# Kernel tuning notes

Hardware: AMD Instinct MI355X
Metric: run time of the kernel (lower is better)

## Reference

```python
import jax, jax.numpy as jnp
import numpy as np

NUM_EXPERTS = 8
NUM_SLOTS = 4

def setup_inputs() -> dict:
    key = jax.random.key(0)
    k1, k2 = jax.random.split(key)
    B, S, D = 8, 4096, 1024
    x = jax.random.normal(k1, (B, S, D), dtype=jnp.float32)
    W_phi = jax.random.normal(k2, (D, NUM_EXPERTS * NUM_SLOTS), dtype=jnp.float32) * (1.0 / np.sqrt(D))
    b_phi = jnp.zeros((NUM_EXPERTS * NUM_SLOTS,), dtype=jnp.float32)
    return {"x": x, "W_phi": W_phi, "b_phi": b_phi}

def reference(x, W_phi, b_phi):
    B, S, D = x.shape
    E, P = NUM_EXPERTS, NUM_SLOTS
    # phi logits: (B, S, E, P)
    phi_logits = (jnp.einsum('bsd,dk->bsk', x, W_phi) + b_phi).reshape(B, S, E, P)
    # softmax over seq axis (dispatch weights)
    phi_weights = jax.nn.softmax(phi_logits, axis=1)
    # soft slots: weighted sum of tokens per (expert, slot) -> (B, E, P, D)
    # (faithful to expand_dims*multiply*sum-over-seq in the original, fused as einsum)
    soft_slots = jnp.einsum('bsep,bsd->bepd', phi_weights, x)
    expert_inputs = soft_slots.reshape(B, E, P * D)
    expert_weights = jnp.full((B, S, E), 1.0 / E, dtype=x.dtype)
    expert_indices = jnp.broadcast_to(jnp.arange(E, dtype=jnp.int32)[None, None, :], (B, S, E))
    raw_gate_probs = jax.nn.softmax(phi_logits, axis=-1)
    return (expert_weights, expert_indices, phi_weights, soft_slots, expert_inputs, phi_logits, raw_gate_probs)
```

## Files before the change

kernel.cpp:

```cpp
#include <hip/hip_runtime.h>
#include <hip/hip_bf16.h>

#define BB 8
#define SS 4096
#define DD 1024
#define KK 32
#define EE 8
#define PP 4

#define O0 0L
#define O1 262144L
#define O2 524288L
#define O3 1572864L
#define O4 1835008L
#define O5 2097152L
#define O6 3145728L

#define WA 0L
#define WB 8192L
#define WPKH 16384L
#define WPKL 32768L
#define WC 49152L

typedef __attribute__((ext_vector_type(8))) short short8v;
typedef __attribute__((ext_vector_type(4))) float f32x4;

__device__ __forceinline__ unsigned short f2bf(float f) {
    unsigned u = __builtin_bit_cast(unsigned, f);
    unsigned r = (u + 0x7FFFu + ((u >> 16) & 1u)) >> 16;
    return (unsigned short)r;
}
__device__ __forceinline__ float bf2f(unsigned short h) {
    return __builtin_bit_cast(float, (unsigned)h << 16);
}

__global__ __launch_bounds__(256) void k_wprep(const float* __restrict__ Wp,
    unsigned short* __restrict__ wh, unsigned short* __restrict__ wl)
{
    const int t  = blockIdx.x * 256 + threadIdx.x;
    const int l  = t & 63;
    const int tt = (t >> 6) & 1;
    const int ks = t >> 7;
    const int col = tt * 16 + (l & 15);
    const int dbase = ks * 32 + (l >> 4) * 8;
    const long obase = ((long)(ks * 2 + tt) * 64 + l) * 8;
#pragma unroll
    for (int j = 0; j < 8; ++j) {
        const float w = Wp[(long)(dbase + j) * KK + col];
        const unsigned short h = f2bf(w);
        const float lo = w - bf2f(h);
        wh[obase + j] = h;
        wl[obase + j] = f2bf(lo);
    }
}

__global__ __launch_bounds__(256) void k_logits_mfma(const float* __restrict__ x,
    const unsigned short* __restrict__ wh, const unsigned short* __restrict__ wl,
    float* __restrict__ wsP)
{
    const int tid  = threadIdx.x;
    const int wv   = tid >> 6;
    const int lane = tid & 63;
    const int blk  = blockIdx.x;
    const int tile = blk >> 1, half = blk & 1;
    const long tokw = (long)tile * 64 + wv * 16;
    const int mrow = lane & 15;
    const int kg   = lane >> 4;

    const float* xr = x + (tokw + mrow) * DD + half * 512 + kg * 8;
    const uint4* bh = reinterpret_cast<const uint4*>(wh) + (long)half * 16 * 2 * 64 + lane;
    const uint4* bl = reinterpret_cast<const uint4*>(wl) + (long)half * 16 * 2 * 64 + lane;

    f32x4 acc0 = {0.f, 0.f, 0.f, 0.f};
    f32x4 acc1 = {0.f, 0.f, 0.f, 0.f};

#pragma unroll 4
    for (int s = 0; s < 16; ++s) {
        const float4 u0 = *reinterpret_cast<const float4*>(xr + s * 32);
        const float4 u1 = *reinterpret_cast<const float4*>(xr + s * 32 + 4);
        const short8v b0h = __builtin_bit_cast(short8v, bh[(long)(s * 2    ) * 64]);
        const short8v b1h = __builtin_bit_cast(short8v, bh[(long)(s * 2 + 1) * 64]);
        const short8v b0l = __builtin_bit_cast(short8v, bl[(long)(s * 2    ) * 64]);
        const short8v b1l = __builtin_bit_cast(short8v, bl[(long)(s * 2 + 1) * 64]);

        const float xf[8] = {u0.x, u0.y, u0.z, u0.w, u1.x, u1.y, u1.z, u1.w};
        short8v ah, al;
#pragma unroll
        for (int j = 0; j < 8; ++j) {
            const unsigned short h = f2bf(xf[j]);
            ah[j] = (short)h;
            al[j] = (short)f2bf(xf[j] - bf2f(h));
        }
        acc0 = __builtin_amdgcn_mfma_f32_16x16x32_bf16(ah, b0h, acc0, 0, 0, 0);
        acc1 = __builtin_amdgcn_mfma_f32_16x16x32_bf16(ah, b1h, acc1, 0, 0, 0);
        acc0 = __builtin_amdgcn_mfma_f32_16x16x32_bf16(al, b0h, acc0, 0, 0, 0);
        acc1 = __builtin_amdgcn_mfma_f32_16x16x32_bf16(al, b1h, acc1, 0, 0, 0);
        acc0 = __builtin_amdgcn_mfma_f32_16x16x32_bf16(ah, b0l, acc0, 0, 0, 0);
        acc1 = __builtin_amdgcn_mfma_f32_16x16x32_bf16(ah, b1l, acc1, 0, 0, 0);
    }

#pragma unroll
    for (int r = 0; r < 4; ++r) {
        const long tok = tokw + kg * 4 + r;
        float* o = wsP + ((long)half * 32768 + tok) * KK + mrow;
        o[0]  = acc0[r];
        o[16] = acc1[r];
    }
}

__global__ __launch_bounds__(256) void k_comb2(const float* __restrict__ wsP,
    const float* __restrict__ bp, float* __restrict__ out, float* __restrict__ ws)
{
    const int blk = blockIdx.x;
    const int tid = threadIdx.x;
    const int wv  = __builtin_amdgcn_readfirstlane(tid >> 6);
    const long g  = (long)blk * 256 + tid;
    float acc[KK];
#pragma unroll
    for (int k = 0; k < KK; ++k) acc[k] = bp[k];
#pragma unroll
    for (int h = 0; h < 2; ++h) {
        const float4* p = reinterpret_cast<const float4*>(wsP + ((long)h * 32768 + g) * KK);
#pragma unroll
        for (int m = 0; m < 8; ++m) {
            const float4 v = p[m];
            acc[4*m]   += v.x;
            acc[4*m+1] += v.y;
            acc[4*m+2] += v.z;
            acc[4*m+3] += v.w;
        }
    }
    float4* pl = reinterpret_cast<float4*>(out + O5 + g * KK);
#pragma unroll
    for (int m = 0; m < 8; ++m)
        pl[m] = make_float4(acc[4*m], acc[4*m+1], acc[4*m+2], acc[4*m+3]);
    float rg[KK];
#pragma unroll
    for (int e = 0; e < EE; ++e) {
        const float mx = fmaxf(fmaxf(acc[4*e], acc[4*e+1]), fmaxf(acc[4*e+2], acc[4*e+3]));
        float s = 0.f;
#pragma unroll
        for (int p = 0; p < PP; ++p) { rg[4*e+p] = __expf(acc[4*e+p] - mx); s += rg[4*e+p]; }
        const float ri = 1.f / s;
#pragma unroll
        for (int p = 0; p < PP; ++p) rg[4*e+p] *= ri;
    }
    float4* prg = reinterpret_cast<float4*>(out + O6 + g * KK);
#pragma unroll
    for (int m = 0; m < 8; ++m)
        prg[m] = make_float4(rg[4*m], rg[4*m+1], rg[4*m+2], rg[4*m+3]);
    float4* pew = reinterpret_cast<float4*>(out + O0 + g * EE);
    pew[0] = make_float4(0.125f, 0.125f, 0.125f, 0.125f);
    pew[1] = make_float4(0.125f, 0.125f, 0.125f, 0.125f);
    float4* pei = reinterpret_cast<float4*>(out + O1 + g * EE);
    pei[0] = make_float4(0.f, 1.f, 2.f, 3.f);
    pei[1] = make_float4(4.f, 5.f, 6.f, 7.f);

    float m[KK];
#pragma unroll
    for (int k = 0; k < KK; ++k) m[k] = acc[k];
    for (int off = 1; off < 64; off <<= 1) {
#pragma unroll
        for (int k = 0; k < KK; ++k) m[k] = fmaxf(m[k], __shfl_xor(m[k], off));
    }
    __shared__ float lm[4][KK];
    __shared__ float lsum[4][KK];
    if ((tid & 63) == 0) {
#pragma unroll
        for (int k = 0; k < KK; ++k) lm[wv][k] = m[k];
    }
    __syncthreads();
#pragma unroll
    for (int k = 0; k < KK; ++k)
        m[k] = fmaxf(fmaxf(lm[0][k], lm[1][k]), fmaxf(lm[2][k], lm[3][k]));
    float sv[KK];
#pragma unroll
    for (int k = 0; k < KK; ++k) sv[k] = __expf(acc[k] - m[k]);
    for (int off = 1; off < 64; off <<= 1) {
#pragma unroll
        for (int k = 0; k < KK; ++k) sv[k] += __shfl_xor(sv[k], off);
    }
    if ((tid & 63) == 0) {
#pragma unroll
        for (int k = 0; k < KK; ++k) lsum[wv][k] = sv[k];
    }
    __syncthreads();
    if (tid == 0) {
#pragma unroll
        for (int k = 0; k < KK; ++k) {
            ws[WA + (long)blk * 64 + k]      = m[k];
            ws[WA + (long)blk * 64 + 32 + k] = lsum[0][k] + lsum[1][k] + lsum[2][k] + lsum[3][k];
        }
    }
}

__global__ __launch_bounds__(256) void k_logits4(const float* __restrict__ x,
    const float* __restrict__ Wp, const float* __restrict__ bp,
    float* __restrict__ out)
{
    __shared__ float xl[2][64][68];
    __shared__ float wl[2][64][32];
    const int tid  = threadIdx.x;
    const int wv   = __builtin_amdgcn_readfirstlane(tid >> 6);
    const int lane = tid & 63;
    const long tok0 = (long)blockIdx.x * 64;
    const long g   = tok0 + lane;
    const int sr = tid >> 2;
    const int sco = (tid & 3) * 4;
    float acc[8];
#pragma unroll
    for (int j = 0; j < 8; ++j) acc[j] = 0.f;
    float4 xr[4], wr[2];
#pragma unroll
    for (int j = 0; j < 4; ++j)
        xr[j] = *reinterpret_cast<const float4*>(x + (tok0 + sr) * DD + sco + j * 16);
#pragma unroll
    for (int j = 0; j < 2; ++j)
        wr[j] = *reinterpret_cast<const float4*>(Wp + tid * 8 + j * 4);
#pragma unroll
    for (int j = 0; j < 4; ++j)
        *reinterpret_cast<float4*>(&xl[0][sr][sco + j * 16]) = xr[j];
#pragma unroll
    for (int j = 0; j < 2; ++j)
        *reinterpret_cast<float4*>(&wl[0][0][0] + tid * 8 + j * 4) = wr[j];
    __syncthreads();
    for (int c = 0; c < 16; ++c) {
        const int cb = c & 1;
        if (c < 15) {
            const long dg = (long)(c + 1) * 64;
#pragma unroll
            for (int j = 0; j < 4; ++j)
                xr[j] = *reinterpret_cast<const float4*>(
                    x + (tok0 + sr) * DD + dg + sco + j * 16);
#pragma unroll
            for (int j = 0; j < 2; ++j)
                wr[j] = *reinterpret_cast<const float4*>(Wp + dg * KK + tid * 8 + j * 4);
        }
        const float* xb = &xl[cb][lane][0];
        const float* wb = &wl[cb][0][0] + wv * 8;
#pragma unroll 4
        for (int dq = 0; dq < 16; ++dq) {
            const float4 xv = *reinterpret_cast<const float4*>(xb + dq * 4);
#pragma unroll
            for (int dd = 0; dd < 4; ++dd) {
                const float xs = (dd == 0) ? xv.x : (dd == 1) ? xv.y
                               : (dd == 2) ? xv.z : xv.w;
                const float4 w0 = *reinterpret_cast<const float4*>(wb + (dq * 4 + dd) * 32);
                const float4 w1 = *reinterpret_cast<const float4*>(wb + (dq * 4 + dd) * 32 + 4);
                acc[0] = fmaf(xs, w0.x, acc[0]);
                acc[1] = fmaf(xs, w0.y, acc[1]);
                acc[2] = fmaf(xs, w0.z, acc[2]);
                acc[3] = fmaf(xs, w0.w, acc[3]);
                acc[4] = fmaf(xs, w1.x, acc[4]);
                acc[5] = fmaf(xs, w1.y, acc[5]);
                acc[6] = fmaf(xs, w1.z, acc[6]);
                acc[7] = fmaf(xs, w1.w, acc[7]);
            }
        }
        if (c < 15) {
#pragma unroll
            for (int j = 0; j < 4; ++j)
                *reinterpret_cast<float4*>(&xl[cb ^ 1][sr][sco + j * 16]) = xr[j];
#pragma unroll
            for (int j = 0; j < 2; ++j)
                *reinterpret_cast<float4*>(&wl[cb ^ 1][0][0] + tid * 8 + j * 4) = wr[j];
        }
        __syncthreads();
    }
#pragma unroll
    for (int j = 0; j < 8; ++j) acc[j] += bp[wv * 8 + j];
    float* o5 = out + O5 + g * KK + wv * 8;
    *reinterpret_cast<float4*>(o5)     = make_float4(acc[0], acc[1], acc[2], acc[3]);
    *reinterpret_cast<float4*>(o5 + 4) = make_float4(acc[4], acc[5], acc[6], acc[7]);
    float rg[8];
#pragma unroll
    for (int e = 0; e < 2; ++e) {
        const float* aa = &acc[e * 4];
        const float m = fmaxf(fmaxf(aa[0], aa[1]), fmaxf(aa[2], aa[3]));
        float s = 0.f;
#pragma unroll
        for (int p = 0; p < PP; ++p) { rg[e*4+p] = __expf(aa[p] - m); s += rg[e*4+p]; }
        const float ri = 1.f / s;
#pragma unroll
        for (int p = 0; p < PP; ++p) rg[e*4+p] *= ri;
    }
    float* o6 = out + O6 + g * KK + wv * 8;
    *reinterpret_cast<float4*>(o6)     = make_float4(rg[0], rg[1], rg[2], rg[3]);
    *reinterpret_cast<float4*>(o6 + 4) = make_float4(rg[4], rg[5], rg[6], rg[7]);
    if (wv == 0) {
        float4* p = reinterpret_cast<float4*>(out + O0 + g * EE);
        p[0] = make_float4(0.125f, 0.125f, 0.125f, 0.125f);
        p[1] = make_float4(0.125f, 0.125f, 0.125f, 0.125f);
    } else if (wv == 1) {
        float4* p = reinterpret_cast<float4*>(out + O1 + g * EE);
        p[0] = make_float4(0.f, 1.f, 2.f, 3.f);
        p[1] = make_float4(4.f, 5.f, 6.f, 7.f);
    }
}

__global__ __launch_bounds__(256) void k_smpart(const float* __restrict__ out,
                                                float* __restrict__ ws)
{
    const int blk = blockIdx.x;
    const int tid = threadIdx.x;
    const int wv  = __builtin_amdgcn_readfirstlane(tid >> 6);
    const int b = blk >> 4, sc = blk & 15;
    const long s  = (long)sc * 256 + tid;
    const float* row = out + O5 + ((long)b * SS + s) * KK;
    float v[KK];
    const float4* r4 = reinterpret_cast<const float4*>(row);
#pragma unroll
    for (int q = 0; q < 8; ++q) {
        const float4 t = r4[q];
        v[4*q] = t.x; v[4*q+1] = t.y; v[4*q+2] = t.z; v[4*q+3] = t.w;
    }
    float m[KK];
#pragma unroll
    for (int k = 0; k < KK; ++k) m[k] = v[k];
    for (int off = 1; off < 64; off <<= 1) {
#pragma unroll
        for (int k = 0; k < KK; ++k) m[k] = fmaxf(m[k], __shfl_xor(m[k], off));
    }
    __shared__ float lm[4][KK];
    __shared__ float lsum[4][KK];
    if ((tid & 63) == 0) {
#pragma unroll
        for (int k = 0; k < KK; ++k) lm[wv][k] = m[k];
    }
    __syncthreads();
#pragma unroll
    for (int k = 0; k < KK; ++k)
        m[k] = fmaxf(fmaxf(lm[0][k], lm[1][k]), fmaxf(lm[2][k], lm[3][k]));
    float sv[KK];
#pragma unroll
    for (int k = 0; k < KK; ++k) sv[k] = __expf(v[k] - m[k]);
    for (int off = 1; off < 64; off <<= 1) {
#pragma unroll
        for (int k = 0; k < KK; ++k) sv[k] += __shfl_xor(sv[k], off);
    }
    if ((tid & 63) == 0) {
#pragma unroll
        for (int k = 0; k < KK; ++k) lsum[wv][k] = sv[k];
    }
    __syncthreads();
    if (tid == 0) {
#pragma unroll
        for (int k = 0; k < KK; ++k) {
            ws[WA + (long)blk * 64 + k]      = m[k];
            ws[WA + (long)blk * 64 + 32 + k] = lsum[0][k] + lsum[1][k] + lsum[2][k] + lsum[3][k];
        }
    }
}

__global__ __launch_bounds__(256) void k_smcomb(float* __restrict__ ws)
{
    const int tid = threadIdx.x;
    const int b = tid >> 5, k = tid & 31;
    float m = -1e30f, s = 0.f;
    for (int c = 0; c < 16; ++c) {
        const float mc = ws[WA + (long)(b * 16 + c) * 64 + k];
        const float sc = ws[WA + (long)(b * 16 + c) * 64 + 32 + k];
        const float nm = fmaxf(m, mc);
        s = s * __expf(m - nm) + sc * __expf(mc - nm);
        m = nm;
    }
    ws[WB + (long)b * 64 + k]      = m;
    ws[WB + (long)b * 64 + 32 + k] = 1.f / s;
}

__global__ __launch_bounds__(256) void k_slots2pw(const float* __restrict__ x,
    float* __restrict__ out, const float* __restrict__ ws,
    float* __restrict__ dst, int SC, int SLEN)
{
    __shared__ float pwl[2][64 * KK];
    const int tid = threadIdx.x;
    const int blk = blockIdx.x;
    const int sc  = blk % SC;
    const int t2  = blk / SC;
    const int dc  = t2 & 3;
    const int b   = t2 >> 2;
    const int d   = dc * 256 + tid;
    const int k0  = (tid & 3) * 8;

    float km[8], krv[8];
#pragma unroll
    for (int j = 0; j < 8; ++j) {
        km[j]  = ws[WB + (long)b * 64 + k0 + j];
        krv[j] = ws[WB + (long)b * 64 + 32 + k0 + j];
    }

    float acc[KK];
#pragma unroll
    for (int k = 0; k < KK; ++k) acc[k] = 0.f;
    const long s0 = (long)sc * SLEN;
    const float* lg = out + O5 + ((long)b * SS + s0) * KK;
    float* o2       = out + O2 + ((long)b * SS + s0) * KK;
    const float* xp = x + ((long)b * SS + s0) * DD + d;
    const int NCH = SLEN >> 6;

    float4 r0 = *reinterpret_cast<const float4*>(lg + tid * 8);
    float4 r1 = *reinterpret_cast<const float4*>(lg + tid * 8 + 4);
    {
        const float4 t0 = make_float4(__expf(r0.x - km[0]) * krv[0],
                                      __expf(r0.y - km[1]) * krv[1],
                                      __expf(r0.z - km[2]) * krv[2],
                                      __expf(r0.w - km[3]) * krv[3]);
        const float4 t1 = make_float4(__expf(r1.x - km[4]) * krv[4],
                                      __expf(r1.y - km[5]) * krv[5],
                                      __expf(r1.z - km[6]) * krv[6],
                                      __expf(r1.w - km[7]) * krv[7]);
        *reinterpret_cast<float4*>(&pwl[0][tid * 8])     = t0;
        *reinterpret_cast<float4*>(&pwl[0][tid * 8 + 4]) = t1;
        if (dc == 0) {
            *reinterpret_cast<float4*>(o2 + tid * 8)     = t0;
            *reinterpret_cast<float4*>(o2 + tid * 8 + 4) = t1;
        }
    }
    __syncthreads();

    for (int ch = 0; ch < NCH; ++ch) {
        const int cb = ch & 1;
        if (ch + 1 < NCH) {
            const float* ln = lg + (long)(ch + 1) * 64 * KK;
            r0 = *reinterpret_cast<const float4*>(ln + tid * 8);
            r1 = *reinterpret_cast<const float4*>(ln + tid * 8 + 4);
        }
        const float* xc = xp + (long)ch * 64 * DD;
        const float* pb = &pwl[cb][0];
#pragma unroll 8
        for (int i = 0; i < 64; ++i) {
            const float xv = xc[(long)i * DD];
#pragma unroll
            for (int q = 0; q < 8; ++q) {
                const float4 w = *reinterpret_cast<const float4*>(pb + i * KK + q * 4);
                acc[4*q]   = fmaf(w.x, xv, acc[4*q]);
                acc[4*q+1] = fmaf(w.y, xv, acc[4*q+1]);
                acc[4*q+2] = fmaf(w.z, xv, acc[4*q+2]);
                acc[4*q+3] = fmaf(w.w, xv, acc[4*q+3]);
            }
        }
        if (ch + 1 < NCH) {
            const float4 t0 = make_float4(__expf(r0.x - km[0]) * krv[0],
                                          __expf(r0.y - km[1]) * krv[1],
                                          __expf(r0.z - km[2]) * krv[2],
                                          __expf(r0.w - km[3]) * krv[3]);
            const float4 t1 = make_float4(__expf(r1.x - km[4]) * krv[4],
                                          __expf(r1.y - km[5]) * krv[5],
                                          __expf(r1.z - km[6]) * krv[6],
                                          __expf(r1.w - km[7]) * krv[7]);
            *reinterpret_cast<float4*>(&pwl[cb ^ 1][tid * 8])     = t0;
            *reinterpret_cast<float4*>(&pwl[cb ^ 1][tid * 8 + 4]) = t1;
            if (dc == 0) {
                float* on = o2 + (long)(ch + 1) * 64 * KK;
                *reinterpret_cast<float4*>(on + tid * 8)     = t0;
                *reinterpret_cast<float4*>(on + tid * 8 + 4) = t1;
            }
        }
        __syncthreads();
    }
    float* o = dst + ((long)(sc * BB + b) * KK) * DD + d;
#pragma unroll
    for (int k = 0; k < KK; ++k) o[(long)k * DD] = acc[k];
}

__global__ __launch_bounds__(256) void k_red(const float* __restrict__ src,
                                             float* __restrict__ out, int SC)
{
    const long i4 = (long)blockIdx.x * 256 + threadIdx.x;
    float4 s = make_float4(0.f, 0.f, 0.f, 0.f);
    const float4* p = reinterpret_cast<const float4*>(src);
    for (int c = 0; c < SC; ++c) {
        const float4 t = p[(long)c * 65536 + i4];
        s.x += t.x; s.y += t.y; s.z += t.z; s.w += t.w;
    }
    reinterpret_cast<float4*>(out + O3)[i4] = s;
    reinterpret_cast<float4*>(out + O4)[i4] = s;
}

extern "C" void kernel_launch(void* const* d_in, const int* in_sizes, int n_in,
                              void* d_out, int out_size, void* d_ws, size_t ws_size,
                              hipStream_t stream)
{
    const float* x  = (const float*)d_in[0];
    const float* Wp = (const float*)d_in[1];
    const float* bp = (const float*)d_in[2];
    float* out = (float*)d_out;
    float* ws  = (float*)d_ws;

    const size_t wfloats = ws_size / 4;
    const long wsP_floats = 2L * 32768 * KK;
    const bool mfma_ok = wfloats >= (size_t)(WC + wsP_floats);

    if (mfma_ok) {
        unsigned short* wh = (unsigned short*)(ws + WPKH);
        unsigned short* wl = (unsigned short*)(ws + WPKL);
        hipLaunchKernelGGL(k_wprep,       dim3(16),   dim3(256), 0, stream, Wp, wh, wl);
        hipLaunchKernelGGL(k_logits_mfma, dim3(1024), dim3(256), 0, stream, x, wh, wl, ws + WC);
        hipLaunchKernelGGL(k_comb2,       dim3(128),  dim3(256), 0, stream, ws + WC, bp, out, ws);
    } else {
        hipLaunchKernelGGL(k_logits4, dim3(512), dim3(256), 0, stream, x, Wp, bp, out);
        hipLaunchKernelGGL(k_smpart,  dim3(128), dim3(256), 0, stream, out, ws);
    }

    hipLaunchKernelGGL(k_smcomb, dim3(1), dim3(256), 0, stream, ws);

    int SC = 0;
    if      (wfloats >= (size_t)(WC + 16L * 262144)) SC = 16;
    else if (wfloats >= (size_t)(WC +  8L * 262144)) SC = 8;
    else if (wfloats >= (size_t)(WC +  4L * 262144)) SC = 4;
    else if (wfloats >= (size_t)(WC +  2L * 262144)) SC = 2;
    else if (wfloats >= (size_t)(WC +  1L * 262144)) SC = 1;

    if (SC >= 1) {
        hipLaunchKernelGGL(k_slots2pw, dim3(BB * 4 * SC), dim3(256), 0, stream,
                           x, out, ws, ws + WC, SC, SS / SC);
        hipLaunchKernelGGL(k_red, dim3(256), dim3(256), 0, stream, ws + WC, out, SC);
    } else {
        hipLaunchKernelGGL(k_slots2pw, dim3(BB * 4), dim3(256), 0, stream,
                           x, out, ws, out + O3, 1, SS);
        hipLaunchKernelGGL(k_red, dim3(256), dim3(256), 0, stream, out + O3, out, 1);
    }
}
```

Baseline: 108.7 us.

## Compute soft-slot weighted sums with split-bf16 MFMA using prepacked phi-weight fragments

Adds a kernel that finishes the sequence softmax, writes phi_weights, and packs them into hi/lo bf16 MFMA fragment layouts. A new slots kernel then computes the weighted token sums with 16x16x32 bf16 MFMAs, using a three-term hi/lo split to keep near-fp32 accuracy. This replaces the scalar FMA slots kernel and the single-block softmax-combine kernel on the main path. The cost is an extra fragment-pack pass, more workspace, and three MFMA products per tile, with some risk of accuracy loss.

```diff
diff --git a/kernel.cpp b/kernel.cpp
--- a/kernel.cpp
+++ b/kernel.cpp
@@ -20,7 +20,9 @@
 #define WB 8192L
 #define WPKH 16384L
 #define WPKL 32768L
-#define WC 49152L
+#define PWFH 49152L
+#define PWFL 573440L
+#define WC2 1097728L
 
 typedef __attribute__((ext_vector_type(8))) short short8v;
 typedef __attribute__((ext_vector_type(4))) float f32x4;
@@ -192,6 +194,125 @@
             ws[WA + (long)blk * 64 + 32 + k] = lsum[0][k] + lsum[1][k] + lsum[2][k] + lsum[3][k];
         }
     }
+}
+
+__global__ __launch_bounds__(256) void k_pwfrag(float* __restrict__ out,
+    const float* __restrict__ ws, unsigned short* __restrict__ fh,
+    unsigned short* __restrict__ fl)
+{
+    const int blk = blockIdx.x;
+    const int b  = blk >> 7;
+    const int t  = threadIdx.x;
+    const int h  = t >> 7;
+    const int l  = (t >> 1) & 63;
+    const int jh = t & 1;
+    const int k  = h * 16 + (l & 15);
+    const long sbase = (long)(blk & 127) * 32 + ((l >> 4) << 3) + jh * 4;
+
+    float m = -1e30f, s = 0.f;
+#pragma unroll
+    for (int c = 0; c < 16; ++c) {
+        const float mc = ws[WA + (long)(b * 16 + c) * 64 + k];
+        const float sc = ws[WA + (long)(b * 16 + c) * 64 + 32 + k];
+        const float nm = fmaxf(m, mc);
+        s = s * __expf(m - nm) + sc * __expf(mc - nm);
+        m = nm;
+    }
+    const float rv = 1.f / s;
+
+    unsigned short hh[4], ll[4];
+#pragma unroll
+    for (int j2 = 0; j2 < 4; ++j2) {
+        const long sg = (long)b * SS + sbase + j2;
+        const float lg = out[O5 + sg * KK + k];
+        const float pw = __expf(lg - m) * rv;
+        out[O2 + sg * KK + k] = pw;
+        const unsigned u = __builtin_bit_cast(unsigned, pw);
+        hh[j2] = (unsigned short)(u >> 16);
+        const float hi = __builtin_bit_cast(float, u & 0xFFFF0000u);
+        ll[j2] = (unsigned short)(__builtin_bit_cast(unsigned, pw - hi) >> 16);
+    }
+    const long fb = (((long)blk * 2 + h) * 64 + l) * 8 + jh * 4;
+    *reinterpret_cast<uint2*>(fh + fb) =
+        make_uint2((unsigned)hh[0] | ((unsigned)hh[1] << 16),
+                   (unsigned)hh[2] | ((unsigned)hh[3] << 16));
+    *reinterpret_cast<uint2*>(fl + fb) =
+        make_uint2((unsigned)ll[0] | ((unsigned)ll[1] << 16),
+                   (unsigned)ll[2] | ((unsigned)ll[3] << 16));
+}
+
+__global__ __launch_bounds__(256) void k_slots_mfma(const float* __restrict__ x,
+    const unsigned short* __restrict__ fh, const unsigned short* __restrict__ fl,
+    float* __restrict__ dst, int SC, int SLEN)
+{
+    const int tid  = threadIdx.x;
+    const int wv   = tid >> 6;
+    const int lane = tid & 63;
+    const int blk  = blockIdx.x;
+    const int sc   = blk % SC;
+    const int t2   = blk / SC;
+    const int dt   = t2 & 15;
+    const int b    = t2 >> 4;
+    const int d0   = dt * 64 + wv * 16;
+    const int n    = lane & 15;
+    const int kg   = lane >> 4;
+    const int CPS  = SLEN >> 5;
+
+    const float* xb = x + ((long)b * SS + (long)sc * SLEN) * DD + d0 + n;
+    const uint4* FH = reinterpret_cast<const uint4*>(fh);
+    const uint4* FL = reinterpret_cast<const uint4*>(fl);
+
+    f32x4 a0 = {0.f, 0.f, 0.f, 0.f};
+    f32x4 a1 = {0.f, 0.f, 0.f, 0.f};
+
+#pragma unroll 2
+    for (int c = 0; c < CPS; ++c) {
+        float xf[8];
+#pragma unroll
+        for (int j = 0; j < 8; ++j)
+            xf[j] = xb[(long)(c * 32 + kg * 8 + j) * DD];
+        short8v xh, xl;
+#pragma unroll
+        for (int j = 0; j < 8; ++j) {
+            const unsigned u = __builtin_bit_cast(unsigned, xf[j]);
+            xh[j] = (short)(u >> 16);
+            const float hi = __builtin_bit_cast(float, u & 0xFFFF0000u);
+            xl[j] = (short)(__builtin_bit_cast(unsigned, xf[j] - hi) >> 16);
+        }
+        const long fidx = ((long)(b * 128 + sc * CPS + c) * 2) * 64 + lane;
+        const short8v p0h = __builtin_bit_cast(short8v, FH[fidx]);
+        const short8v p0l = __builtin_bit_cast(short8v, FL[fidx]);
+        const short8v p1h = __builtin_bit_cast(short8v, FH[fidx + 64]);
+        const short8v p1l = __builtin_bit_cast(short8v, FL[fidx + 64]);
+
+        a0 = __builtin_amdgcn_mfma_f32_16x16x32_bf16(p0h, xh, a0, 0, 0, 0);
+        a1 = __builtin_amdgcn_mfma_f32_16x16x32_bf16(p1h, xh, a1, 0, 0, 0);
+        a0 = __builtin_amdgcn_mfma_f32_16x16x32_bf16(p0l, xh, a0, 0, 0, 0);
+        a1 = __builtin_amdgcn_mfma_f32_16x16x32_bf16(p1l, xh, a1, 0, 0, 0);
+        a0 = __builtin_amdgcn_mfma_f32_16x16x32_bf16(p0h, xl, a0, 0, 0, 0);
+        a1 = __builtin_amdgcn_mfma_f32_16x16x32_bf16(p1h, xl, a1, 0, 0, 0);
+    }
+
+    float* ob = dst + ((long)(sc * BB + b) * KK) * DD + d0 + n;
+#pragma unroll
+    for (int r = 0; r < 4; ++r) {
+        ob[(long)((kg << 2) + r) * DD]        = a0[r];
+        ob[(long)(16 + (kg << 2) + r) * DD]   = a1[r];
+    }
+}
+
+__global__ __launch_bounds__(256) void k_red(const float* __restrict__ src,
+                                             float* __restrict__ out, int SC)
+{
+    const long i4 = (long)blockIdx.x * 256 + threadIdx.x;
+    float4 s = make_float4(0.f, 0.f, 0.f, 0.f);
+    const float4* p = reinterpret_cast<const float4*>(src);
+    for (int c = 0; c < SC; ++c) {
+        const float4 t = p[(long)c * 65536 + i4];
+        s.x += t.x; s.y += t.y; s.z += t.z; s.w += t.w;
+    }
+    reinterpret_cast<float4*>(out + O3)[i4] = s;
+    reinterpret_cast<float4*>(out + O4)[i4] = s;
 }
 
 __global__ __launch_bounds__(256) void k_logits4(const float* __restrict__ x,
@@ -463,20 +584,6 @@
     for (int k = 0; k < KK; ++k) o[(long)k * DD] = acc[k];
 }
 
-__global__ __launch_bounds__(256) void k_red(const float* __restrict__ src,
-                                             float* __restrict__ out, int SC)
-{
-    const long i4 = (long)blockIdx.x * 256 + threadIdx.x;
-    float4 s = make_float4(0.f, 0.f, 0.f, 0.f);
-    const float4* p = reinterpret_cast<const float4*>(src);
-    for (int c = 0; c < SC; ++c) {
-        const float4 t = p[(long)c * 65536 + i4];
-        s.x += t.x; s.y += t.y; s.z += t.z; s.w += t.w;
-    }
-    reinterpret_cast<float4*>(out + O3)[i4] = s;
-    reinterpret_cast<float4*>(out + O4)[i4] = s;
-}
-
 extern "C" void kernel_launch(void* const* d_in, const int* in_sizes, int n_in,
                               void* d_out, int out_size, void* d_ws, size_t ws_size,
                               hipStream_t stream)
@@ -488,36 +595,38 @@
     float* ws  = (float*)d_ws;
 
     const size_t wfloats = ws_size / 4;
-    const long wsP_floats = 2L * 32768 * KK;
-    const bool mfma_ok = wfloats >= (size_t)(WC + wsP_floats);
+    const long need = WC2 + 2L * 32768 * KK;
+    const bool mfma_ok = wfloats >= (size_t)need;
 
     if (mfma_ok) {
         unsigned short* wh = (unsigned short*)(ws + WPKH);
         unsigned short* wl = (unsigned short*)(ws + WPKL);
+        unsigned short* fh = (unsigned short*)(ws + PWFH);
+        unsigned short* fl = (unsigned short*)(ws + PWFL);
         hipLaunchKernelGGL(k_wprep,       dim3(16),   dim3(256), 0, stream, Wp, wh, wl);
-        hipLaunchKernelGGL(k_logits_mfma, dim3(1024), dim3(256), 0, stream, x, wh, wl, ws + WC);
-        hipLaunchKernelGGL(k_comb2,       dim3(128),  dim3(256), 0, stream, ws + WC, bp, out, ws);
+        hipLaunchKernelGGL(k_logits_mfma, dim3(1024), dim3(256), 0, stream, x, wh, wl, ws + WC2);
+        hipLaunchKernelGGL(k_comb2,       dim3(128),  dim3(256), 0, stream, ws + WC2, bp, out, ws);
+        hipLaunchKernelGGL(k_pwfrag,      dim3(1024), dim3(256), 0, stream, out, ws, fh, fl);
+        hipLaunchKernelGGL(k_slots_mfma,  dim3(BB * 16 * 8), dim3(256), 0, stream,
+                           x, fh, fl, ws + WC2, 8, SS / 8);
+        hipLaunchKernelGGL(k_red,         dim3(256),  dim3(256), 0, stream, ws + WC2, out, 8);
     } else {
         hipLaunchKernelGGL(k_logits4, dim3(512), dim3(256), 0, stream, x, Wp, bp, out);
         hipLaunchKernelGGL(k_smpart,  dim3(128), dim3(256), 0, stream, out, ws);
-    }
-
-    hipLaunchKernelGGL(k_smcomb, dim3(1), dim3(256), 0, stream, ws);
-
-    int SC = 0;
-    if      (wfloats >= (size_t)(WC + 16L * 262144)) SC = 16;
-    else if (wfloats >= (size_t)(WC +  8L * 262144)) SC = 8;
-    else if (wfloats >= (size_t)(WC +  4L * 262144)) SC = 4;
-    else if (wfloats >= (size_t)(WC +  2L * 262144)) SC = 2;
-    else if (wfloats >= (size_t)(WC +  1L * 262144)) SC = 1;
-
-    if (SC >= 1) {
-        hipLaunchKernelGGL(k_slots2pw, dim3(BB * 4 * SC), dim3(256), 0, stream,
-                           x, out, ws, ws + WC, SC, SS / SC);
-        hipLaunchKernelGGL(k_red, dim3(256), dim3(256), 0, stream, ws + WC, out, SC);
-    } else {
-        hipLaunchKernelGGL(k_slots2pw, dim3(BB * 4), dim3(256), 0, stream,
-                           x, out, ws, out + O3, 1, SS);
-        hipLaunchKernelGGL(k_red, dim3(256), dim3(256), 0, stream, out + O3, out, 1);
-    }
-}
+        hipLaunchKernelGGL(k_smcomb,  dim3(1),   dim3(256), 0, stream, ws);
+        int SC = 0;
+        if      (wfloats >= (size_t)(WC2 + 8L * 262144)) SC = 8;
+        else if (wfloats >= (size_t)(WC2 + 4L * 262144)) SC = 4;
+        else if (wfloats >= (size_t)(WC2 + 2L * 262144)) SC = 2;
+        else if (wfloats >= (size_t)(WC2 + 1L * 262144)) SC = 1;
+        if (SC >= 1) {
+            hipLaunchKernelGGL(k_slots2pw, dim3(BB * 4 * SC), dim3(256), 0, stream,
+                               x, out, ws, ws + WC2, SC, SS / SC);
+            hipLaunchKernelGGL(k_red, dim3(256), dim3(256), 0, stream, ws + WC2, out, SC);
+        } else {
+            hipLaunchKernelGGL(k_slots2pw, dim3(BB * 4), dim3(256), 0, stream,
+                               x, out, ws, out + O3, 1, SS);
+            hipLaunchKernelGGL(k_red, dim3(256), dim3(256), 0, stream, out + O3, out, 1);
+        }
+    }
+}
```

After: 87.39 us, median of 2. 1.24x faster.
